# Optimization experiments

Measured on AMD Instinct MI355X. Metric: run time of the kernel, lower is better.

Reference implementation:

```python
import jax, jax.numpy as jnp
import numpy as np


def setup_inputs() -> dict:
    key = jax.random.key(0)
    k1, k2, k3 = jax.random.split(key, 3)
    B, C, H, W = 8, 256, 128, 128
    x = jax.random.normal(k1, (B, C, H, W), dtype=jnp.float32)
    # 1x1 conv: Conv2d(5C -> C), weight stored as [C_out, 5C]
    fan_in = 5 * C
    bound = 1.0 / np.sqrt(fan_in)
    conv_w = jax.random.uniform(k2, (C, 5 * C), dtype=jnp.float32, minval=-bound, maxval=bound)
    conv_b = jax.random.uniform(k3, (C,), dtype=jnp.float32, minval=-bound, maxval=bound)
    return {"x": x, "conv_w": conv_w, "conv_b": conv_b}


def reference(x, conv_w, conv_b):
    # Directional prefix/suffix max.
    # up_to_bottom: cumulative max along H (top->bottom)
    x1 = jax.lax.cummax(x, axis=2)
    # bottom_to_up: suffix max along H
    x2 = jax.lax.cummax(x, axis=2, reverse=True)
    # left_to_right (rot90 trick in torch) == cumulative max along W
    x3 = jax.lax.cummax(x, axis=3)
    # right_to_left == suffix max along W
    x4 = jax.lax.cummax(x, axis=3, reverse=True)
    x_con = jnp.concatenate((x, x1, x2, x3, x4), axis=1)  # [B, 5C, H, W]
    # 1x1 conv == channel contraction
    out = jnp.einsum('bchw,oc->bohw', x_con, conv_w) + conv_b[None, :, None, None]
    return out
```

## Files before the change

### kernel.cpp

```cpp
#include <hip/hip_runtime.h>
#include <stdint.h>


#define N_  131072
#define K_  1280

typedef unsigned short ushort8v __attribute__((ext_vector_type(8)));
typedef unsigned short ushort4v __attribute__((ext_vector_type(4)));
typedef short          short8v  __attribute__((ext_vector_type(8)));
typedef float          float4v  __attribute__((ext_vector_type(4)));

__device__ __forceinline__ unsigned short f2bf(float f) {
    unsigned int u = __builtin_bit_cast(unsigned int, f);
    u += 0x7fffu + ((u >> 16) & 1u);
    return (unsigned short)(u >> 16);
}

__device__ __forceinline__ void load_lds16(const void* g, void* l) {
    __builtin_amdgcn_global_load_lds(
        (const __attribute__((address_space(1))) uint32_t*)g,
        (__attribute__((address_space(3))) uint32_t*)l,
        16, 0, 0);
}

__global__ void repack_w(const float* __restrict__ w, unsigned short* __restrict__ wsA) {
    int idx = blockIdx.x * 256 + threadIdx.x;
    float4 v = ((const float4*)w)[idx];
    int m = idx / 320;
    int k = (idx - m * 320) << 2;
    ushort4v o = { f2bf(v.x), f2bf(v.y), f2bf(v.z), f2bf(v.w) };
    *(ushort4v*)(wsA + ((size_t)(k >> 3) << 11) + (m << 3) + (k & 7)) = o;
}

__global__ __launch_bounds__(256) void scan_h(const float* __restrict__ x,
                                              unsigned short* __restrict__ wsB) {
    int idx = blockIdx.x;
    int wq = idx & 3, cb = (idx >> 2) & 31, b = idx >> 7;
    int t = threadIdx.x;
    int j = t >> 5, wi = t & 31;
    const float* src = x + (((size_t)(b * 256 + cb * 8 + j)) << 14) + wq * 32 + wi;
    unsigned short* d0 = wsB + (((size_t)(cb)      * N_) << 3);
    unsigned short* d1 = wsB + (((size_t)(32 + cb) * N_) << 3);
    unsigned short* d2 = wsB + (((size_t)(64 + cb) * N_) << 3);
    size_t nbase = ((size_t)b << 14) + wq * 32;

    __shared__ unsigned short sm0[16 * 32 * 8];
    __shared__ unsigned short sm1[16 * 32 * 8];

    float r = -INFINITY;
    for (int hb = 0; hb < 8; ++hb) {
        int h0 = hb << 4;
#pragma unroll
        for (int hh = 0; hh < 16; ++hh) {
            float v = src[(size_t)(h0 + hh) << 7];
            r = fmaxf(r, v);
            sm0[((hh << 5) + wi) * 8 + j] = f2bf(v);
            sm1[((hh << 5) + wi) * 8 + j] = f2bf(r);
        }
        __syncthreads();
#pragma unroll
        for (int k = 0; k < 2; ++k) {
            int p = t + (k << 8);
            int hh = p >> 5, wo = p & 31;
            size_t n = nbase + (size_t)(h0 + hh) * 128 + wo;
            ushort8v a = *(const ushort8v*)(sm0 + (((hh << 5) + wo) << 3));
            ushort8v c = *(const ushort8v*)(sm1 + (((hh << 5) + wo) << 3));
            *(ushort8v*)(d0 + (n << 3)) = a;
            *(ushort8v*)(d1 + (n << 3)) = c;
        }
        __syncthreads();
    }
    r = -INFINITY;
    for (int hb = 7; hb >= 0; --hb) {
        int h0 = hb << 4;
#pragma unroll
        for (int hh = 15; hh >= 0; --hh) {
            float v = src[(size_t)(h0 + hh) << 7];
            r = fmaxf(r, v);
            sm0[((hh << 5) + wi) * 8 + j] = f2bf(r);
        }
        __syncthreads();
#pragma unroll
        for (int k = 0; k < 2; ++k) {
            int p = t + (k << 8);
            int hh = p >> 5, wo = p & 31;
            size_t n = nbase + (size_t)(h0 + hh) * 128 + wo;
            *(ushort8v*)(d2 + (n << 3)) = *(const ushort8v*)(sm0 + (((hh << 5) + wo) << 3));
        }
        __syncthreads();
    }
}

__global__ __launch_bounds__(256) void scan_w(const float* __restrict__ x,
                                              unsigned short* __restrict__ wsB) {
    int idx = blockIdx.x;
    int hq = idx & 3, cb = (idx >> 2) & 31, b = idx >> 7;
    int t = threadIdx.x;
    int j = t >> 5, hh = t & 31;
    (void)j; (void)hh;

    __shared__ float xs[16][260];
    __shared__ unsigned short po[32][136];

    const float* xb = x + (((size_t)(b * 256 + cb * 8)) << 14) + ((size_t)(hq * 32) << 7);
    unsigned short* d3 = wsB + (((size_t)(96  + cb) * N_) << 3);
    unsigned short* d4 = wsB + (((size_t)(128 + cb) * N_) << 3);
    size_t nrow0 = ((size_t)b << 14) + (size_t)(hq * 32) * 128;

    {
        float r = -INFINITY;
        for (int wc = 0; wc < 8; ++wc) {
#pragma unroll
            for (int k = 0; k < 4; ++k) {
                int f = t + (k << 8);
                int row = f >> 2, pos = f & 3;
                float4 v = *(const float4*)(xb + ((size_t)(row >> 5) << 14) +
                                            ((row & 31) << 7) + (wc << 4) + (pos << 2));
                xs[pos * 4 + 0][row] = v.x; xs[pos * 4 + 1][row] = v.y;
                xs[pos * 4 + 2][row] = v.z; xs[pos * 4 + 3][row] = v.w;
            }
            __syncthreads();
#pragma unroll
            for (int w = 0; w < 16; ++w) {
                r = fmaxf(r, xs[w][t]);
                po[t & 31][w * 8 + (t >> 5)] = f2bf(r);
            }
            __syncthreads();
#pragma unroll
            for (int k = 0; k < 2; ++k) {
                int p = t + (k << 8);
                int ph = p >> 4, pw = p & 15;
                size_t n = nrow0 + (size_t)ph * 128 + (wc << 4) + pw;
                *(ushort8v*)(d3 + (n << 3)) = *(const ushort8v*)(&po[ph][pw << 3]);
            }
            __syncthreads();
        }
    }
    {
        float r = -INFINITY;
        for (int wc = 7; wc >= 0; --wc) {
#pragma unroll
            for (int k = 0; k < 4; ++k) {
                int f = t + (k << 8);
                int row = f >> 2, pos = f & 3;
                float4 v = *(const float4*)(xb + ((size_t)(row >> 5) << 14) +
                                            ((row & 31) << 7) + (wc << 4) + (pos << 2));
                xs[pos * 4 + 0][row] = v.x; xs[pos * 4 + 1][row] = v.y;
                xs[pos * 4 + 2][row] = v.z; xs[pos * 4 + 3][row] = v.w;
            }
            __syncthreads();
#pragma unroll
            for (int w = 15; w >= 0; --w) {
                r = fmaxf(r, xs[w][t]);
                po[t & 31][w * 8 + (t >> 5)] = f2bf(r);
            }
            __syncthreads();
#pragma unroll
            for (int k = 0; k < 2; ++k) {
                int p = t + (k << 8);
                int ph = p >> 4, pw = p & 15;
                size_t n = nrow0 + (size_t)ph * 128 + (wc << 4) + pw;
                *(ushort8v*)(d4 + (n << 3)) = *(const ushort8v*)(&po[ph][pw << 3]);
            }
            __syncthreads();
        }
    }
}


__device__ __forceinline__ void stage_tile(
    const unsigned short* __restrict__ wsA, const unsigned short* __restrict__ wsB,
    int t, int n0, unsigned short* As, unsigned short* Bs, int tid) {
    const unsigned short* ga = wsA + ((((size_t)t << 11) + tid) << 3);
#pragma unroll
    for (int r = 0; r < 4; ++r)
        load_lds16(ga + (r << 12), As + (((r << 9) + tid) << 3));
    int kb0 = t << 3;
#pragma unroll
    for (int r = 0; r < 4; ++r) {
        int idx = (r << 9) + tid;
        load_lds16(wsB + (((size_t)(kb0 + (idx >> 8)) * N_ + n0 + (idx & 255)) << 3),
                   Bs + ((size_t)idx << 3));
    }
}

__device__ __forceinline__ void compute_tile(
    const unsigned short* __restrict__ Ab, const unsigned short* __restrict__ Bb,
    int wr, int wc, int q, int lr, float4v (&acc)[8][4]) {
#pragma unroll
    for (int h = 0; h < 2; ++h) {
        short8v a[8], bb[4];
        int kq = (h << 2) + q;
#pragma unroll
        for (int mi = 0; mi < 8; ++mi)
            a[mi] = *(const short8v*)(Ab + (((kq << 8) + (wr << 7) + (mi << 4) + lr) << 3));
#pragma unroll
        for (int ni = 0; ni < 4; ++ni)
            bb[ni] = *(const short8v*)(Bb + (((kq << 8) + (wc << 6) + (ni << 4) + lr) << 3));
        __builtin_amdgcn_s_setprio(1);
#pragma unroll
        for (int mi = 0; mi < 8; ++mi)
#pragma unroll
            for (int ni = 0; ni < 4; ++ni)
                acc[mi][ni] = __builtin_amdgcn_mfma_f32_16x16x32_bf16(a[mi], bb[ni], acc[mi][ni], 0, 0, 0);
        __builtin_amdgcn_s_setprio(0);
    }
}

__global__ __launch_bounds__(512, 2) void gemm_k(
    const unsigned short* __restrict__ wsA, const unsigned short* __restrict__ wsB,
    const float* __restrict__ bias, float* __restrict__ out) {
    __shared__ __align__(16) unsigned short As[2][16384];
    __shared__ __align__(16) unsigned short Bs[2][16384];

    int tid  = threadIdx.x;
    int lane = tid & 63, wid = tid >> 6;
    int wr = wid >> 2, wc = wid & 3;
    int q  = lane >> 4, lr = lane & 15;
    int bid = blockIdx.x;
    int n0 = (((bid & 7) << 6) + (bid >> 3)) << 8;

    float4v acc[8][4];
#pragma unroll
    for (int mi = 0; mi < 8; ++mi)
#pragma unroll
        for (int ni = 0; ni < 4; ++ni)
            acc[mi][ni] = (float4v){0.f, 0.f, 0.f, 0.f};

    stage_tile(wsA, wsB, 0, n0, As[0], Bs[0], tid);
    stage_tile(wsA, wsB, 1, n0, As[1], Bs[1], tid);
    asm volatile("s_waitcnt vmcnt(8)" ::: "memory");
    __builtin_amdgcn_s_barrier();
    __builtin_amdgcn_sched_barrier(0);

#pragma unroll 1
    for (int t = 0; t < 18; t += 2) {
        compute_tile(As[0], Bs[0], wr, wc, q, lr, acc);
        __builtin_amdgcn_s_barrier();
        __builtin_amdgcn_sched_barrier(0);
        stage_tile(wsA, wsB, t + 2, n0, As[0], Bs[0], tid);
        __builtin_amdgcn_sched_barrier(0);
        asm volatile("s_waitcnt vmcnt(8)" ::: "memory");
        __builtin_amdgcn_s_barrier();
        __builtin_amdgcn_sched_barrier(0);

        compute_tile(As[1], Bs[1], wr, wc, q, lr, acc);
        __builtin_amdgcn_s_barrier();
        __builtin_amdgcn_sched_barrier(0);
        stage_tile(wsA, wsB, t + 3, n0, As[1], Bs[1], tid);
        __builtin_amdgcn_sched_barrier(0);
        asm volatile("s_waitcnt vmcnt(8)" ::: "memory");
        __builtin_amdgcn_s_barrier();
        __builtin_amdgcn_sched_barrier(0);
    }
    compute_tile(As[0], Bs[0], wr, wc, q, lr, acc);
    __builtin_amdgcn_s_barrier();
    asm volatile("s_waitcnt vmcnt(0)" ::: "memory");
    __builtin_amdgcn_s_barrier();
    __builtin_amdgcn_sched_barrier(0);
    compute_tile(As[1], Bs[1], wr, wc, q, lr, acc);

#pragma unroll
    for (int mi = 0; mi < 8; ++mi) {
        int rowb = (wr << 7) + (mi << 4) + (q << 2);
#pragma unroll
        for (int ni = 0; ni < 4; ++ni) {
            int col = n0 + (wc << 6) + (ni << 4) + lr;
            int b   = col >> 14, p = col & 16383;
            float* op = out + ((size_t)((b << 8) + rowb) << 14) + p;
#pragma unroll
            for (int r = 0; r < 4; ++r)
                op[(size_t)r << 14] = acc[mi][ni][r] + bias[rowb + r];
        }
    }
}

extern "C" void kernel_launch(void* const* d_in, const int* in_sizes, int n_in,
                              void* d_out, int out_size, void* d_ws, size_t ws_size,
                              hipStream_t stream) {
    const float* x  = (const float*)d_in[0];
    const float* cw = (const float*)d_in[1];
    const float* cb = (const float*)d_in[2];
    float* out = (float*)d_out;

    unsigned short* wsA = (unsigned short*)d_ws;
    unsigned short* wsB = wsA + 327680;

    repack_w<<<320, 256, 0, stream>>>(cw, wsA);
    scan_h<<<1024, 256, 0, stream>>>(x, wsB);
    scan_w<<<1024, 256, 0, stream>>>(x, wsB);
    gemm_k<<<512, 512, 0, stream>>>(wsA, wsB, cb, out);
}
```

Measured before the change: 458.0 us.

## Stage input tiles in LDS once per block for both directional scan kernels

Both scan kernels now copy their whole input tile into LDS with asynchronous global-to-LDS loads. The forward and reverse scans then read from LDS instead of fetching x from global memory twice. scan_h waits on staged vmcnt counts so compute can start while later rows are still arriving. scan_w switches to an XOR-swizzled LDS layout to avoid bank conflicts. The roughly 128KB of LDS per block limits each CU to one block, which reduces latency hiding.

```diff
diff --git a/kernel.cpp b/kernel.cpp
--- a/kernel.cpp
+++ b/kernel.cpp
@@ -22,6 +22,8 @@
         (__attribute__((address_space(3))) uint32_t*)l,
         16, 0, 0);
 }
+
+#define WTV(n) asm volatile("s_waitcnt vmcnt(" #n ")" ::: "memory")
 
 __global__ void repack_w(const float* __restrict__ w, unsigned short* __restrict__ wsA) {
     int idx = blockIdx.x * 256 + threadIdx.x;
@@ -37,25 +39,50 @@
     int idx = blockIdx.x;
     int wq = idx & 3, cb = (idx >> 2) & 31, b = idx >> 7;
     int t = threadIdx.x;
-    int j = t >> 5, wi = t & 31;
-    const float* src = x + (((size_t)(b * 256 + cb * 8 + j)) << 14) + wq * 32 + wi;
+    int w0 = t >> 6, lane = t & 63;
+    int c = t >> 5, wi = t & 31;
+
+    __shared__ float xs[8 * 128 * 32];
+    __shared__ unsigned short sm0[16 * 32 * 8];
+    __shared__ unsigned short sm1[16 * 32 * 8];
+
+    const float* xb = x + (((size_t)(b * 256 + cb * 8)) << 14) + wq * 32;
+
+    {
+        int hh = lane >> 3, w4 = lane & 7;
+#pragma unroll
+        for (int r = 0; r < 32; ++r) {
+            int cc = (w0 << 1) + (r & 1);
+            int h0 = (r >> 1) << 3;
+            const float* g = xb + ((size_t)cc << 14) + (size_t)(h0 + hh) * 128 + (w4 << 2);
+            load_lds16(g, (char*)(xs + ((cc << 7) + h0) * 32) + lane * 16);
+        }
+    }
+
     unsigned short* d0 = wsB + (((size_t)(cb)      * N_) << 3);
     unsigned short* d1 = wsB + (((size_t)(32 + cb) * N_) << 3);
     unsigned short* d2 = wsB + (((size_t)(64 + cb) * N_) << 3);
     size_t nbase = ((size_t)b << 14) + wq * 32;
 
-    __shared__ unsigned short sm0[16 * 32 * 8];
-    __shared__ unsigned short sm1[16 * 32 * 8];
-
     float r = -INFINITY;
+#pragma unroll
     for (int hb = 0; hb < 8; ++hb) {
+        if      (hb == 0) WTV(28);
+        else if (hb == 1) WTV(24);
+        else if (hb == 2) WTV(20);
+        else if (hb == 3) WTV(16);
+        else if (hb == 4) WTV(12);
+        else if (hb == 5) WTV(8);
+        else if (hb == 6) WTV(4);
+        else              WTV(0);
+        __builtin_amdgcn_sched_barrier(0);
         int h0 = hb << 4;
 #pragma unroll
         for (int hh = 0; hh < 16; ++hh) {
-            float v = src[(size_t)(h0 + hh) << 7];
+            float v = xs[((c << 7) + h0 + hh) * 32 + wi];
             r = fmaxf(r, v);
-            sm0[((hh << 5) + wi) * 8 + j] = f2bf(v);
-            sm1[((hh << 5) + wi) * 8 + j] = f2bf(r);
+            sm0[(((hh << 5) + wi) << 3) + c] = f2bf(v);
+            sm1[(((hh << 5) + wi) << 3) + c] = f2bf(r);
         }
         __syncthreads();
 #pragma unroll
@@ -63,21 +90,21 @@
             int p = t + (k << 8);
             int hh = p >> 5, wo = p & 31;
             size_t n = nbase + (size_t)(h0 + hh) * 128 + wo;
-            ushort8v a = *(const ushort8v*)(sm0 + (((hh << 5) + wo) << 3));
-            ushort8v c = *(const ushort8v*)(sm1 + (((hh << 5) + wo) << 3));
-            *(ushort8v*)(d0 + (n << 3)) = a;
-            *(ushort8v*)(d1 + (n << 3)) = c;
+            *(ushort8v*)(d0 + (n << 3)) = *(const ushort8v*)(sm0 + (((hh << 5) + wo) << 3));
+            *(ushort8v*)(d1 + (n << 3)) = *(const ushort8v*)(sm1 + (((hh << 5) + wo) << 3));
         }
         __syncthreads();
     }
+
     r = -INFINITY;
+#pragma unroll
     for (int hb = 7; hb >= 0; --hb) {
         int h0 = hb << 4;
 #pragma unroll
         for (int hh = 15; hh >= 0; --hh) {
-            float v = src[(size_t)(h0 + hh) << 7];
+            float v = xs[((c << 7) + h0 + hh) * 32 + wi];
             r = fmaxf(r, v);
-            sm0[((hh << 5) + wi) * 8 + j] = f2bf(r);
+            sm0[(((hh << 5) + wi) << 3) + c] = f2bf(r);
         }
         __syncthreads();
 #pragma unroll
@@ -96,71 +123,87 @@
     int idx = blockIdx.x;
     int hq = idx & 3, cb = (idx >> 2) & 31, b = idx >> 7;
     int t = threadIdx.x;
-    int j = t >> 5, hh = t & 31;
-    (void)j; (void)hh;
-
-    __shared__ float xs[16][260];
-    __shared__ unsigned short po[32][136];
+    int w0 = t >> 6, lane = t & 63;
+    int c = t & 7, h = t >> 3;
+
+    __shared__ float xs[256 * 128];
+    __shared__ unsigned short po[16 * 32 * 8];
 
     const float* xb = x + (((size_t)(b * 256 + cb * 8)) << 14) + ((size_t)(hq * 32) << 7);
+
+    {
+        int rsel = lane >> 5, gp = lane & 31;
+#pragma unroll
+        for (int r = 0; r < 32; ++r) {
+            int cc  = r >> 2;
+            int rs0 = (cc << 5) + (w0 << 3) + ((r & 3) << 1);
+            int row = rs0 + rsel;
+            int gl  = gp ^ (row & 7);
+            const float* g = xb + ((size_t)cc << 14) + ((size_t)(row & 31) << 7) + (gl << 2);
+            load_lds16(g, (char*)(xs + (rs0 << 7)) + lane * 16);
+        }
+    }
+    WTV(0);
+    __builtin_amdgcn_sched_barrier(0);
+
     unsigned short* d3 = wsB + (((size_t)(96  + cb) * N_) << 3);
     unsigned short* d4 = wsB + (((size_t)(128 + cb) * N_) << 3);
     size_t nrow0 = ((size_t)b << 14) + (size_t)(hq * 32) * 128;
+    int rs = (c << 5) + h;
+    int sw = rs & 7;
 
     {
-        float r = -INFINITY;
+        float rr = -INFINITY;
+#pragma unroll
         for (int wc = 0; wc < 8; ++wc) {
 #pragma unroll
-            for (int k = 0; k < 4; ++k) {
-                int f = t + (k << 8);
-                int row = f >> 2, pos = f & 3;
-                float4 v = *(const float4*)(xb + ((size_t)(row >> 5) << 14) +
-                                            ((row & 31) << 7) + (wc << 4) + (pos << 2));
-                xs[pos * 4 + 0][row] = v.x; xs[pos * 4 + 1][row] = v.y;
-                xs[pos * 4 + 2][row] = v.z; xs[pos * 4 + 3][row] = v.w;
+            for (int g = 0; g < 4; ++g) {
+                int l = (wc << 2) + g;
+                float4v v = *(const float4v*)(xs + (rs << 7) + ((l ^ sw) << 2));
+#pragma unroll
+                for (int e = 0; e < 4; ++e) {
+                    rr = fmaxf(rr, v[e]);
+                    int wloc = (g << 2) + e;
+                    int G = (wloc << 5) + h;
+                    po[((G ^ (wloc & 7)) << 3) + c] = f2bf(rr);
+                }
             }
             __syncthreads();
 #pragma unroll
-            for (int w = 0; w < 16; ++w) {
-                r = fmaxf(r, xs[w][t]);
-                po[t & 31][w * 8 + (t >> 5)] = f2bf(r);
+            for (int k = 0; k < 2; ++k) {
+                int p = t + (k << 8);
+                int ww = p & 15, hh = p >> 4;
+                int G = (ww << 5) + hh;
+                size_t n = nrow0 + (size_t)hh * 128 + (wc << 4) + ww;
+                *(ushort8v*)(d3 + (n << 3)) = *(const ushort8v*)(po + ((G ^ (ww & 7)) << 3));
             }
             __syncthreads();
+        }
+    }
+    {
+        float rr = -INFINITY;
+#pragma unroll
+        for (int wc = 7; wc >= 0; --wc) {
+#pragma unroll
+            for (int g = 3; g >= 0; --g) {
+                int l = (wc << 2) + g;
+                float4v v = *(const float4v*)(xs + (rs << 7) + ((l ^ sw) << 2));
+#pragma unroll
+                for (int e = 3; e >= 0; --e) {
+                    rr = fmaxf(rr, v[e]);
+                    int wloc = (g << 2) + e;
+                    int G = (wloc << 5) + h;
+                    po[((G ^ (wloc & 7)) << 3) + c] = f2bf(rr);
+                }
+            }
+            __syncthreads();
 #pragma unroll
             for (int k = 0; k < 2; ++k) {
                 int p = t + (k << 8);
-                int ph = p >> 4, pw = p & 15;
-                size_t n = nrow0 + (size_t)ph * 128 + (wc << 4) + pw;
-                *(ushort8v*)(d3 + (n << 3)) = *(const ushort8v*)(&po[ph][pw << 3]);
-            }
-            __syncthreads();
-        }
-    }
-    {
-        float r = -INFINITY;
-        for (int wc = 7; wc >= 0; --wc) {
-#pragma unroll
-            for (int k = 0; k < 4; ++k) {
-                int f = t + (k << 8);
-                int row = f >> 2, pos = f & 3;
-                float4 v = *(const float4*)(xb + ((size_t)(row >> 5) << 14) +
-                                            ((row & 31) << 7) + (wc << 4) + (pos << 2));
-                xs[pos * 4 + 0][row] = v.x; xs[pos * 4 + 1][row] = v.y;
-                xs[pos * 4 + 2][row] = v.z; xs[pos * 4 + 3][row] = v.w;
-            }
-            __syncthreads();
-#pragma unroll
-            for (int w = 15; w >= 0; --w) {
-                r = fmaxf(r, xs[w][t]);
-                po[t & 31][w * 8 + (t >> 5)] = f2bf(r);
-            }
-            __syncthreads();
-#pragma unroll
-            for (int k = 0; k < 2; ++k) {
-                int p = t + (k << 8);
-                int ph = p >> 4, pw = p & 15;
-                size_t n = nrow0 + (size_t)ph * 128 + (wc << 4) + pw;
-                *(ushort8v*)(d4 + (n << 3)) = *(const ushort8v*)(&po[ph][pw << 3]);
+                int ww = p & 15, hh = p >> 4;
+                int G = (ww << 5) + hh;
+                size_t n = nrow0 + (size_t)hh * 128 + (wc << 4) + ww;
+                *(ushort8v*)(d4 + (n << 3)) = *(const ushort8v*)(po + ((G ^ (ww & 7)) << 3));
             }
             __syncthreads();
         }
@@ -289,5 +332,5 @@
     repack_w<<<320, 256, 0, stream>>>(cw, wsA);
     scan_h<<<1024, 256, 0, stream>>>(x, wsB);
     scan_w<<<1024, 256, 0, stream>>>(x, wsB);
-    gemm_k<<<512, 512, 0, stream>>>(wsA, wsB, cb, out);
-}
+    gemm_k<<<dim3(512), 512, 0, stream>>>(wsA, wsB, cb, out);
+}
```

Measured after the change: 439.5 us. -4.0%, faster.
